# Kernel optimization log

Measured on AMD Instinct MI355X. Metric: run time of the kernel, lower is better.

## Reference

```python
import jax, jax.numpy as jnp
import numpy as np

B, N, E1, H, D = 16, 256, 4, 8, 128  # batch, max nodes, edge types+1, heads, dim
VOCAB = 100


def setup_inputs() -> dict:
    key = jax.random.key(0)
    ks = jax.random.split(key, 20)
    s = 0.05
    return dict(
        node_feat=jax.random.randint(ks[0], (B, N), 0, VOCAB),
        L=jax.random.normal(ks[1], (B, N, N, E1), jnp.float32),
        emb=jax.random.normal(ks[2], (VOCAB, D), jnp.float32) * s,
        W0=jax.random.normal(ks[3], (E1, H, D, D), jnp.float32) * s,
        W1=jax.random.normal(ks[4], (E1, H, D * H * E1, D), jnp.float32) * (s / 4.0),
        a1w0=jax.random.normal(ks[5], (E1, H, D), jnp.float32) * s,
        a1b0=jnp.zeros((E1, H), jnp.float32),
        a2w0=jax.random.normal(ks[6], (E1, H, D), jnp.float32) * s,
        a2b0=jnp.zeros((E1, H), jnp.float32),
        a1w1=jax.random.normal(ks[7], (E1, H, D), jnp.float32) * s,
        a1b1=jnp.zeros((E1, H), jnp.float32),
        a2w1=jax.random.normal(ks[8], (E1, H, D), jnp.float32) * s,
        a2b1=jnp.zeros((E1, H), jnp.float32),
        sb0=jnp.zeros((E1, H, D), jnp.float32),
        sb1=jnp.zeros((E1, H, D), jnp.float32),
        outW=jax.random.normal(ks[9], (D, D), jnp.float32) * s,
        outb=jnp.zeros((D,), jnp.float32),
        attW=jax.random.normal(ks[10], (D,), jnp.float32) * s,
        attb=jnp.zeros((), jnp.float32),
    )


def _gat_layer(state, Ltr, W, a1w, a1b, a2w, a2b, sb, last):
    # state: (B, N, Din); W: (E1, H, Din, D); Ltr: (E1, 1, B, N, N)
    Wh = jnp.einsum('bni,ehio->ehbno', state, W)                      # (E1,H,B,N,D)
    s1 = jnp.einsum('ehbno,eho->ehbn', Wh, a1w) + a1b[:, :, None, None]
    s2 = jnp.einsum('ehbno,eho->ehbn', Wh, a2w) + a2b[:, :, None, None]
    logits = jax.nn.leaky_relu(s1[..., :, None] + s2[..., None, :], 0.2) + Ltr
    att = jax.nn.softmax(logits, axis=3)  # torch softmax over dim=1 of (B,N,N)
    h = jnp.einsum('ehbnm,ehbmo->ehbno', att, Wh) + sb[:, :, None, None, :]
    if last:
        return jnp.mean(h, axis=(0, 1))                               # (B,N,D)
    h = jax.nn.elu(h)
    # concat order in torch: outer edge-type jj, inner head ii -> (B,N,E1*H*D)
    return jnp.transpose(h, (2, 3, 0, 1, 4)).reshape(state.shape[0], state.shape[1], -1)


def reference(node_feat, L, emb, W0, W1, a1w0, a1b0, a2w0, a2b0,
              a1w1, a1b1, a2w1, a2b1, sb0, sb1, outW, outb, attW, attb):
    Ltr = jnp.transpose(L, (3, 0, 1, 2))[:, None]  # (E1,1,B,N,N)
    state = emb[node_feat]                         # (B,N,D)
    state = _gat_layer(state, Ltr, W0, a1w0, a1b0, a2w0, a2b0, sb0, last=False)
    state = _gat_layer(state, Ltr, W1, a1w1, a1b1, a2w1, a2b1, sb1, last=True)
    y = state @ outW + outb                        # (B,N,D)
    aw = jax.nn.sigmoid(state @ attW + attb)       # (B,N)
    y = aw[..., None] * y
    return jnp.mean(y, axis=1)                     # (B,D)
```

## Files before the change

### kernel.cpp

```cpp
#include <hip/hip_runtime.h>
#include <hip/hip_bf16.h>

#define Bq 16
#define Nq 256
#define E1q 4
#define Hq 8
#define Dq 128
#define EH 32
#define BN 4096

typedef __hip_bfloat16 bf16;
typedef short bf16x8 __attribute__((ext_vector_type(8)));
typedef float f32x4 __attribute__((ext_vector_type(4)));

__device__ __forceinline__ void gll16(const void* gptr, void* lptr) {
    __builtin_amdgcn_global_load_lds(
        (const __attribute__((address_space(1))) void*)gptr,
        (__attribute__((address_space(3))) void*)lptr, 16, 0, 0);
}

__device__ __forceinline__ unsigned short f2bf(float v) {
    __hip_bfloat16 h = __float2bfloat16(v);
    return *(unsigned short*)&h;
}

__global__ __launch_bounds__(256) void gather_kernel(const int* __restrict__ nf,
                                                     const float* __restrict__ emb,
                                                     bf16* __restrict__ st0b) {
    int i = blockIdx.x * 256 + threadIdx.x;
    int row = i >> 7, col = i & 127;
    st0b[i] = __float2bfloat16(emb[nf[row] * Dq + col]);
}

__global__ __launch_bounds__(256) void transpose_kernel(const float* __restrict__ W,
                                                        bf16* __restrict__ WT, int K) {
    int kt = blockIdx.x, nt = blockIdx.y, eh = blockIdx.z;
    __shared__ float tile[64][65];
    int tr = threadIdx.x >> 6, tc = threadIdx.x & 63;
    const float* src = W + ((size_t)eh * K + kt * 64) * 128 + nt * 64;
#pragma unroll
    for (int p = 0; p < 16; ++p) {
        int r = p * 4 + tr;
        tile[r][tc] = src[(size_t)r * 128 + tc];
    }
    __syncthreads();
    bf16* dst = WT + ((size_t)eh * 128 + nt * 64) * K + kt * 64;
#pragma unroll
    for (int p = 0; p < 16; ++p) {
        int n = p * 4 + tr;
        dst[(size_t)n * K + tc] = __float2bfloat16(tile[tc][n]);
    }
}

__global__ __launch_bounds__(256) void pack_le_kernel(const float* __restrict__ L,
                                                      float* __restrict__ Le) {
    int idx = blockIdx.x * 256 + threadIdx.x;
    float4 v = *(const float4*)(L + (size_t)idx * 4);
    Le[idx] = v.x;
    Le[1048576 + idx] = v.y;
    Le[2097152 + idx] = v.z;
    Le[3145728 + idx] = v.w;
}

__global__ __launch_bounds__(256) void mfma_gemm_kernel(const bf16* __restrict__ Ab,
                                                        const bf16* __restrict__ Bt,
                                                        bf16* __restrict__ Wht,
                                                        const float* __restrict__ a1w,
                                                        const float* __restrict__ a1b,
                                                        const float* __restrict__ a2w,
                                                        const float* __restrict__ a2b,
                                                        float* __restrict__ s1,
                                                        float* __restrict__ s2, int K) {
    int rt = blockIdx.x;
    int eh = blockIdx.y;
    int tid = threadIdx.x;
    int w = tid >> 6, l = tid & 63;
    int q = l >> 4, mn = l & 15;
    __shared__ __align__(16) bf16 As[128 * 64];
    __shared__ __align__(16) bf16 Bs[128 * 64];
    __shared__ float red1[128], red2[128];
    const bf16* Ap = Ab + (size_t)(rt * 128) * K;
    const bf16* Bp = Bt + (size_t)eh * 128 * K;
    int lr = l >> 3;
    int g = (l & 7) ^ lr;
    int gcol = g * 8;

    if (tid < 128) { red1[tid] = 0.f; red2[tid] = 0.f; }

    f32x4 acc[4][4];
#pragma unroll
    for (int i = 0; i < 4; i++)
#pragma unroll
        for (int j = 0; j < 4; j++) acc[i][j] = (f32x4){0.f, 0.f, 0.f, 0.f};

    int wr = (w >> 1) * 64, wc = (w & 1) * 64;
    int msw = mn & 7;

    for (int k0 = 0; k0 < K; k0 += 64) {
#pragma unroll
        for (int u = 0; u < 4; ++u) {
            int i = w * 4 + u;
            int r = i * 8 + lr;
            gll16(Ap + (size_t)r * K + k0 + gcol, (char*)As + i * 1024);
            gll16(Bp + (size_t)r * K + k0 + gcol, (char*)Bs + i * 1024);
        }
        __syncthreads();
#pragma unroll
        for (int kk = 0; kk < 2; ++kk) {
            int qb = ((kk * 4 + q) ^ msw) * 16;
            bf16x8 af[4], bfr[4];
#pragma unroll
            for (int i = 0; i < 4; ++i) {
                af[i]  = *(const bf16x8*)((const char*)As + (wr + i * 16 + mn) * 128 + qb);
                bfr[i] = *(const bf16x8*)((const char*)Bs + (wc + i * 16 + mn) * 128 + qb);
            }
#pragma unroll
            for (int i = 0; i < 4; ++i)
#pragma unroll
                for (int j = 0; j < 4; ++j)
                    acc[i][j] = __builtin_amdgcn_mfma_f32_16x16x32_bf16(af[i], bfr[j], acc[i][j], 0, 0, 0);
        }
        __syncthreads();
    }
#pragma unroll
    for (int i = 0; i < 4; ++i) {
        int r0 = rt * 128 + wr + i * 16 + q * 4;
        int b = r0 >> 8, m = r0 & 255;
#pragma unroll
        for (int j = 0; j < 4; ++j) {
            int o = wc + j * 16 + mn;
            ushort4 pk;
            pk.x = f2bf(acc[i][j][0]);
            pk.y = f2bf(acc[i][j][1]);
            pk.z = f2bf(acc[i][j][2]);
            pk.w = f2bf(acc[i][j][3]);
            *(ushort4*)(Wht + ((((size_t)eh * 16 + b) * 128 + o) * 256 + m)) = pk;
        }
    }
    float w1v[4], w2v[4];
#pragma unroll
    for (int j = 0; j < 4; ++j) {
        int o = wc + j * 16 + mn;
        w1v[j] = a1w[eh * 128 + o];
        w2v[j] = a2w[eh * 128 + o];
    }
#pragma unroll
    for (int i = 0; i < 4; ++i)
#pragma unroll
        for (int r = 0; r < 4; ++r) {
            float p1 = 0.f, p2 = 0.f;
#pragma unroll
            for (int j = 0; j < 4; ++j) {
                p1 += acc[i][j][r] * w1v[j];
                p2 += acc[i][j][r] * w2v[j];
            }
#pragma unroll
            for (int off = 1; off < 16; off <<= 1) {
                p1 += __shfl_xor(p1, off);
                p2 += __shfl_xor(p2, off);
            }
            if (mn == 0) {
                int row = wr + i * 16 + q * 4 + r;
                atomicAdd(&red1[row], p1);
                atomicAdd(&red2[row], p2);
            }
        }
    __syncthreads();
    if (tid < 128) {
        int rg = rt * 128 + tid;
        s1[eh * 4096 + rg] = red1[tid] + a1b[eh];
        s2[eh * 4096 + rg] = red2[tid] + a2b[eh];
    }
}

__global__ __launch_bounds__(256) void colsoft_kernel(const float* __restrict__ s1,
                                                      const float* __restrict__ s2,
                                                      const float* __restrict__ Le,
                                                      float* __restrict__ cmax,
                                                      float* __restrict__ cinv) {
    int mt = blockIdx.x, b = blockIdx.y, e = blockIdx.z;
    int t = threadIdx.x;
    __shared__ float Lt[256 * 32];
    __shared__ float s1L[8 * 256];
#pragma unroll
    for (int i = 0; i < 8; ++i) s1L[i * 256 + t] = s1[(e * 8 + i) * 4096 + b * 256 + t];
    const float* Lb = Le + ((size_t)(e * 16 + b) * 256) * 256 + mt * 32;
#pragma unroll
    for (int j = 0; j < 8; ++j) {
        int f = t + 256 * j;
        int n = f >> 3, c4 = (f & 7) * 4;
        *(float4*)(Lt + n * 32 + c4) = *(const float4*)(Lb + (size_t)n * 256 + c4);
    }
    __syncthreads();
    int h = t >> 5, mm = t & 31;
    int m = mt * 32 + mm;
    float s2v = s2[(e * 8 + h) * 4096 + b * 256 + m];
    const float* s1p = s1L + h * 256;
    float mx = -1e30f;
    for (int n = 0; n < 256; ++n) {
        float x = s1p[n] + s2v;
        x = x > 0.f ? x : 0.2f * x;
        x += Lt[n * 32 + mm];
        mx = fmaxf(mx, x);
    }
    float sum = 0.f;
    for (int n = 0; n < 256; ++n) {
        float x = s1p[n] + s2v;
        x = x > 0.f ? x : 0.2f * x;
        x += Lt[n * 32 + mm];
        sum += __expf(x - mx);
    }
    cmax[(e * 8 + h) * 4096 + b * 256 + m] = mx;
    cinv[(e * 8 + h) * 4096 + b * 256 + m] = 1.0f / sum;
}

template <int LAST>
__global__ __launch_bounds__(256) void att_mfma_kernel(const float* __restrict__ s1,
                                                       const float* __restrict__ s2,
                                                       const float* __restrict__ cmax,
                                                       const float* __restrict__ cinv,
                                                       const float* __restrict__ Le,
                                                       const bf16* __restrict__ Wht,
                                                       const float* __restrict__ sb,
                                                       void* __restrict__ outv) {
    int nt = blockIdx.x;
    int b = blockIdx.y;
    int eh = blockIdx.z;
    int e = eh >> 3;
    int tid = threadIdx.x;
    int w = tid >> 6, l = tid & 63;
    int q = l >> 4, mn = l & 15;
    __shared__ __align__(16) bf16 As[128 * 32];
    __shared__ __align__(16) bf16 Bs[128 * 40];
    __shared__ float s1L[128], s2L[256], cmL[256], ciL[256];

    int base = eh * 4096 + b * 256;
    if (tid < 128) s1L[tid] = s1[base + nt * 128 + tid];
    s2L[tid] = s2[base + tid];
    cmL[tid] = cmax[base + tid];
    ciL[tid] = cinv[base + tid];
    __syncthreads();

    const bf16* Whtp = Wht + ((size_t)eh * 16 + b) * 32768;
    int nl = tid >> 1, mh = (tid & 1) * 16;
    const float* Lrow = Le + (((size_t)(e * 16 + b) * 256) + nt * 128 + nl) * 256;
    float s1v = s1L[nl];
    int srow = l >> 2;
    int sq = (l & 3) ^ ((l >> 3) & 3);
    int scol = sq * 8;
    int rsw = ((mn >> 1) & 3) << 3;

    f32x4 acc[4][4];
#pragma unroll
    for (int i = 0; i < 4; i++)
#pragma unroll
        for (int j = 0; j < 4; j++) acc[i][j] = (f32x4){0.f, 0.f, 0.f, 0.f};

    int wr = (w >> 1) * 64, wc = (w & 1) * 64;

    for (int k0 = 0; k0 < 256; k0 += 32) {
#pragma unroll
        for (int u = 0; u < 2; ++u) {
            int i = 2 * w + u;
            gll16(Whtp + (size_t)(i * 16 + srow) * 256 + k0 + scol, (char*)As + i * 1024);
        }
#pragma unroll
        for (int jj = 0; jj < 4; ++jj) {
            int mb = mh + jj * 4;
            float4 lv = *(const float4*)(Lrow + k0 + mb);
            float av[4];
#pragma unroll
            for (int c = 0; c < 4; ++c) {
                int m = k0 + mb + c;
                float x = s1v + s2L[m];
                x = x > 0.f ? x : 0.2f * x;
                x += ((const float*)&lv)[c];
                av[c] = __expf(x - cmL[m]) * ciL[m];
            }
            unsigned int u01 = (unsigned int)f2bf(av[0]) | ((unsigned int)f2bf(av[1]) << 16);
            unsigned int u23 = (unsigned int)f2bf(av[2]) | ((unsigned int)f2bf(av[3]) << 16);
            unsigned int* bp = (unsigned int*)Bs + (nl * 40 + mb) / 2;
            bp[0] = u01;
            bp[1] = u23;
        }
        __syncthreads();
        bf16x8 af[4], bfr[4];
#pragma unroll
        for (int i = 0; i < 4; ++i) {
            af[i]  = *(const bf16x8*)(As + (wr + i * 16 + mn) * 32 + ((q << 3) ^ rsw));
            bfr[i] = *(const bf16x8*)(Bs + (wc + i * 16 + mn) * 40 + q * 8);
        }
#pragma unroll
        for (int i = 0; i < 4; ++i)
#pragma unroll
            for (int j = 0; j < 4; ++j)
                acc[i][j] = __builtin_amdgcn_mfma_f32_16x16x32_bf16(af[i], bfr[j], acc[i][j], 0, 0, 0);
        __syncthreads();
    }
#pragma unroll
    for (int i = 0; i < 4; ++i) {
        int o0 = wr + i * 16 + q * 4;
        float4 sbv = *(const float4*)(sb + eh * 128 + o0);
#pragma unroll
        for (int j = 0; j < 4; ++j) {
            int n = wc + j * 16 + mn;
            float v0 = acc[i][j][0] + sbv.x;
            float v1 = acc[i][j][1] + sbv.y;
            float v2 = acc[i][j][2] + sbv.z;
            float v3 = acc[i][j][3] + sbv.w;
            if (LAST == 0) {
                v0 = v0 > 0.f ? v0 : __expf(v0) - 1.f;
                v1 = v1 > 0.f ? v1 : __expf(v1) - 1.f;
                v2 = v2 > 0.f ? v2 : __expf(v2) - 1.f;
                v3 = v3 > 0.f ? v3 : __expf(v3) - 1.f;
                ushort4 pk = {f2bf(v0), f2bf(v1), f2bf(v2), f2bf(v3)};
                bf16* out = (bf16*)outv;
                *(ushort4*)(out + (size_t)(b * 256 + nt * 128 + n) * 4096 + eh * 128 + o0) = pk;
            } else {
                float4 pk = {v0, v1, v2, v3};
                float* out = (float*)outv;
                *(float4*)(out + ((size_t)eh * 4096 + b * 256 + nt * 128 + n) * 128 + o0) = pk;
            }
        }
    }
}

__global__ __launch_bounds__(256) void reduce_aw_kernel(const float* __restrict__ h2,
                                                        const float* __restrict__ attW,
                                                        const float* __restrict__ attb,
                                                        float* __restrict__ st2,
                                                        float* __restrict__ aw) {
    int t = threadIdx.x;
    int rl = t >> 7, o = t & 127;
    int r = blockIdx.x * 2 + rl;
    float acc = 0.f;
#pragma unroll
    for (int eh = 0; eh < EH; ++eh) acc += h2[((size_t)eh * 4096 + r) * 128 + o];
    acc *= (1.0f / 32.0f);
    st2[(size_t)r * 128 + o] = acc;
    float p = acc * attW[o];
#pragma unroll
    for (int off = 32; off; off >>= 1) p += __shfl_down(p, off);
    __shared__ float part[4];
    if ((t & 63) == 0) part[t >> 6] = p;
    __syncthreads();
    if (t == 0) aw[r] = 1.0f / (1.0f + __expf(-(part[0] + part[1] + attb[0])));
    if (t == 128) aw[r] = 1.0f / (1.0f + __expf(-(part[2] + part[3] + attb[0])));
}

__global__ __launch_bounds__(128) void final_kernel(const float* __restrict__ st2,
                                                    const float* __restrict__ aw,
                                                    const float* __restrict__ outW,
                                                    const float* __restrict__ outb,
                                                    float* __restrict__ out) {
    int b = blockIdx.x;
    int t = threadIdx.x;
    __shared__ float awL[256], zL[128];
    awL[t] = aw[b * 256 + t];
    awL[t + 128] = aw[b * 256 + t + 128];
    __syncthreads();
    float z = 0.f;
    for (int n = 0; n < 256; ++n) z += awL[n] * st2[(size_t)(b * 256 + n) * Dq + t];
    float sa = 0.f;
    for (int n = 0; n < 256; ++n) sa += awL[n];
    zL[t] = z;
    __syncthreads();
    float acc = sa * outb[t];
    for (int o = 0; o < Dq; ++o) acc += zL[o] * outW[o * Dq + t];
    out[b * Dq + t] = acc * (1.0f / 256.0f);
}

extern "C" void kernel_launch(void* const* d_in, const int* in_sizes, int n_in,
                              void* d_out, int out_size, void* d_ws, size_t ws_size,
                              hipStream_t stream) {
    const int* nf = (const int*)d_in[0];
    const float* L = (const float*)d_in[1];
    const float* emb = (const float*)d_in[2];
    const float* W0 = (const float*)d_in[3];
    const float* W1 = (const float*)d_in[4];
    const float* a1w0 = (const float*)d_in[5];
    const float* a1b0 = (const float*)d_in[6];
    const float* a2w0 = (const float*)d_in[7];
    const float* a2b0 = (const float*)d_in[8];
    const float* a1w1 = (const float*)d_in[9];
    const float* a1b1 = (const float*)d_in[10];
    const float* a2w1 = (const float*)d_in[11];
    const float* a2b1 = (const float*)d_in[12];
    const float* sb0 = (const float*)d_in[13];
    const float* sb1 = (const float*)d_in[14];
    const float* outW = (const float*)d_in[15];
    const float* outb = (const float*)d_in[16];
    const float* attW = (const float*)d_in[17];
    const float* attb = (const float*)d_in[18];

    char* p = (char*)d_ws;
    bf16* st0b = (bf16*)(p);
    bf16* W0T  = (bf16*)(p + 1048576);
    bf16* W1T  = (bf16*)(p + 2097152);
    bf16* st1b = (bf16*)(p + 35651584);
    float* h2  = (float*)(p + 2097152);
    float* Le  = (float*)(p + 69206016);
    bf16* Wht  = (bf16*)(p + 85983232);
    float* s1  = (float*)(p + 119537664);
    float* s2  = (float*)(p + 120061952);
    float* cmax= (float*)(p + 120586240);
    float* cinv= (float*)(p + 121110528);
    float* st2 = (float*)(p);
    float* aw  = s1;
    float* outp = (float*)d_out;

    gather_kernel<<<2048, 256, 0, stream>>>(nf, emb, st0b);
    transpose_kernel<<<dim3(2, 2, 32), 256, 0, stream>>>(W0, W0T, 128);
    transpose_kernel<<<dim3(64, 2, 32), 256, 0, stream>>>(W1, W1T, 4096);
    pack_le_kernel<<<4096, 256, 0, stream>>>(L, Le);

    mfma_gemm_kernel<<<dim3(32, 32), 256, 0, stream>>>(st0b, W0T, Wht, a1w0, a1b0, a2w0, a2b0, s1, s2, 128);
    colsoft_kernel<<<dim3(8, 16, 4), 256, 0, stream>>>(s1, s2, Le, cmax, cinv);
    att_mfma_kernel<0><<<dim3(2, 16, 32), 256, 0, stream>>>(s1, s2, cmax, cinv, Le, Wht, sb0, st1b);

    mfma_gemm_kernel<<<dim3(32, 32), 256, 0, stream>>>(st1b, W1T, Wht, a1w1, a1b1, a2w1, a2b1, s1, s2, 4096);
    colsoft_kernel<<<dim3(8, 16, 4), 256, 0, stream>>>(s1, s2, Le, cmax, cinv);
    att_mfma_kernel<1><<<dim3(2, 16, 32), 256, 0, stream>>>(s1, s2, cmax, cinv, Le, Wht, sb1, h2);

    reduce_aw_kernel<<<2048, 256, 0, stream>>>(h2, attW, attb, st2, aw);
    final_kernel<<<16, 128, 0, stream>>>(st2, aw, outW, outb, outp);
}
```

Baseline: 502.1 us.

## Fuse prep kernels, remap GEMM blocks per XCD, pack softmax stats, store h2 in bf16

Merges the gather, two weight transposes and the L repack into one prep kernel to cut launch count. The GEMM grid is flattened and remapped so that blocks sharing the same weight slice land on the same XCD, which should improve L2 reuse. The s2, column max and inverse sum values are packed into one float4 array, replacing three separate loads with one. The second-layer attention output is written as bf16 instead of fp32, halving traffic into the reduction at some loss of precision.

```diff
diff --git a/kernel.cpp b/kernel.cpp
--- a/kernel.cpp
+++ b/kernel.cpp
@@ -24,19 +24,11 @@
     return *(unsigned short*)&h;
 }
 
-__global__ __launch_bounds__(256) void gather_kernel(const int* __restrict__ nf,
-                                                     const float* __restrict__ emb,
-                                                     bf16* __restrict__ st0b) {
-    int i = blockIdx.x * 256 + threadIdx.x;
-    int row = i >> 7, col = i & 127;
-    st0b[i] = __float2bfloat16(emb[nf[row] * Dq + col]);
-}
-
-__global__ __launch_bounds__(256) void transpose_kernel(const float* __restrict__ W,
-                                                        bf16* __restrict__ WT, int K) {
-    int kt = blockIdx.x, nt = blockIdx.y, eh = blockIdx.z;
-    __shared__ float tile[64][65];
-    int tr = threadIdx.x >> 6, tc = threadIdx.x & 63;
+__device__ __forceinline__ void transpose_tile(const float* __restrict__ W,
+                                               bf16* __restrict__ WT, int K,
+                                               int kt, int nt, int eh,
+                                               float (*tile)[65], int tid) {
+    int tr = tid >> 6, tc = tid & 63;
     const float* src = W + ((size_t)eh * K + kt * 64) * 128 + nt * 64;
 #pragma unroll
     for (int p = 0; p < 16; ++p) {
@@ -52,14 +44,36 @@
     }
 }
 
-__global__ __launch_bounds__(256) void pack_le_kernel(const float* __restrict__ L,
-                                                      float* __restrict__ Le) {
-    int idx = blockIdx.x * 256 + threadIdx.x;
-    float4 v = *(const float4*)(L + (size_t)idx * 4);
-    Le[idx] = v.x;
-    Le[1048576 + idx] = v.y;
-    Le[2097152 + idx] = v.z;
-    Le[3145728 + idx] = v.w;
+__global__ __launch_bounds__(256) void prep_kernel(const int* __restrict__ nf,
+                                                   const float* __restrict__ emb,
+                                                   const float* __restrict__ W0,
+                                                   const float* __restrict__ W1,
+                                                   const float* __restrict__ L,
+                                                   bf16* __restrict__ st0b,
+                                                   bf16* __restrict__ W0T,
+                                                   bf16* __restrict__ W1T,
+                                                   float* __restrict__ Le) {
+    int bid = blockIdx.x;
+    int t = threadIdx.x;
+    __shared__ float tile[64][65];
+    if (bid < 2048) {
+        int i = bid * 256 + t;
+        int row = i >> 7, col = i & 127;
+        st0b[i] = __float2bfloat16(emb[nf[row] * Dq + col]);
+    } else if (bid < 2176) {
+        int id2 = bid - 2048;
+        transpose_tile(W0, W0T, 128, id2 & 1, (id2 >> 1) & 1, id2 >> 2, tile, t);
+    } else if (bid < 6272) {
+        int id3 = bid - 2176;
+        transpose_tile(W1, W1T, 4096, id3 & 63, (id3 >> 6) & 1, id3 >> 7, tile, t);
+    } else {
+        int idx = (bid - 6272) * 256 + t;
+        float4 v = *(const float4*)(L + (size_t)idx * 4);
+        Le[idx] = v.x;
+        Le[1048576 + idx] = v.y;
+        Le[2097152 + idx] = v.z;
+        Le[3145728 + idx] = v.w;
+    }
 }
 
 __global__ __launch_bounds__(256) void mfma_gemm_kernel(const bf16* __restrict__ Ab,
@@ -71,8 +85,10 @@
                                                         const float* __restrict__ a2b,
                                                         float* __restrict__ s1,
                                                         float* __restrict__ s2, int K) {
-    int rt = blockIdx.x;
-    int eh = blockIdx.y;
+    int id = blockIdx.x;
+    int xcd = id & 7, slot = id >> 3;
+    int eh = (slot & 3) * 8 + xcd;
+    int rt = slot >> 2;
     int tid = threadIdx.x;
     int w = tid >> 6, l = tid & 63;
     int q = l >> 4, mn = l & 15;
@@ -176,8 +192,7 @@
 __global__ __launch_bounds__(256) void colsoft_kernel(const float* __restrict__ s1,
                                                       const float* __restrict__ s2,
                                                       const float* __restrict__ Le,
-                                                      float* __restrict__ cmax,
-                                                      float* __restrict__ cinv) {
+                                                      float4* __restrict__ stat) {
     int mt = blockIdx.x, b = blockIdx.y, e = blockIdx.z;
     int t = threadIdx.x;
     __shared__ float Lt[256 * 32];
@@ -210,19 +225,17 @@
         x += Lt[n * 32 + mm];
         sum += __expf(x - mx);
     }
-    cmax[(e * 8 + h) * 4096 + b * 256 + m] = mx;
-    cinv[(e * 8 + h) * 4096 + b * 256 + m] = 1.0f / sum;
+    float4 st = {s2v, mx, 1.0f / sum, 0.f};
+    stat[(e * 8 + h) * 4096 + b * 256 + m] = st;
 }
 
 template <int LAST>
 __global__ __launch_bounds__(256) void att_mfma_kernel(const float* __restrict__ s1,
-                                                       const float* __restrict__ s2,
-                                                       const float* __restrict__ cmax,
-                                                       const float* __restrict__ cinv,
+                                                       const float4* __restrict__ stat,
                                                        const float* __restrict__ Le,
                                                        const bf16* __restrict__ Wht,
                                                        const float* __restrict__ sb,
-                                                       void* __restrict__ outv) {
+                                                       bf16* __restrict__ outb) {
     int nt = blockIdx.x;
     int b = blockIdx.y;
     int eh = blockIdx.z;
@@ -232,13 +245,12 @@
     int q = l >> 4, mn = l & 15;
     __shared__ __align__(16) bf16 As[128 * 32];
     __shared__ __align__(16) bf16 Bs[128 * 40];
-    __shared__ float s1L[128], s2L[256], cmL[256], ciL[256];
+    __shared__ float s1L[128];
+    __shared__ __align__(16) float4 stL[256];
 
     int base = eh * 4096 + b * 256;
     if (tid < 128) s1L[tid] = s1[base + nt * 128 + tid];
-    s2L[tid] = s2[base + tid];
-    cmL[tid] = cmax[base + tid];
-    ciL[tid] = cinv[base + tid];
+    stL[tid] = stat[base + tid];
     __syncthreads();
 
     const bf16* Whtp = Wht + ((size_t)eh * 16 + b) * 32768;
@@ -272,10 +284,11 @@
 #pragma unroll
             for (int c = 0; c < 4; ++c) {
                 int m = k0 + mb + c;
-                float x = s1v + s2L[m];
+                float4 stv = stL[m];
+                float x = s1v + stv.x;
                 x = x > 0.f ? x : 0.2f * x;
                 x += ((const float*)&lv)[c];
-                av[c] = __expf(x - cmL[m]) * ciL[m];
+                av[c] = __expf(x - stv.y) * stv.z;
             }
             unsigned int u01 = (unsigned int)f2bf(av[0]) | ((unsigned int)f2bf(av[1]) << 16);
             unsigned int u23 = (unsigned int)f2bf(av[2]) | ((unsigned int)f2bf(av[3]) << 16);
@@ -314,18 +327,16 @@
                 v2 = v2 > 0.f ? v2 : __expf(v2) - 1.f;
                 v3 = v3 > 0.f ? v3 : __expf(v3) - 1.f;
                 ushort4 pk = {f2bf(v0), f2bf(v1), f2bf(v2), f2bf(v3)};
-                bf16* out = (bf16*)outv;
-                *(ushort4*)(out + (size_t)(b * 256 + nt * 128 + n) * 4096 + eh * 128 + o0) = pk;
+                *(ushort4*)(outb + (size_t)(b * 256 + nt * 128 + n) * 4096 + eh * Dq + o0) = pk;
             } else {
-                float4 pk = {v0, v1, v2, v3};
-                float* out = (float*)outv;
-                *(float4*)(out + ((size_t)eh * 4096 + b * 256 + nt * 128 + n) * 128 + o0) = pk;
-            }
-        }
-    }
-}
-
-__global__ __launch_bounds__(256) void reduce_aw_kernel(const float* __restrict__ h2,
+                ushort4 pk = {f2bf(v0), f2bf(v1), f2bf(v2), f2bf(v3)};
+                *(ushort4*)(outb + ((size_t)eh * 4096 + b * 256 + nt * 128 + n) * Dq + o0) = pk;
+            }
+        }
+    }
+}
+
+__global__ __launch_bounds__(256) void reduce_aw_kernel(const bf16* __restrict__ h2b,
                                                         const float* __restrict__ attW,
                                                         const float* __restrict__ attb,
                                                         float* __restrict__ st2,
@@ -335,7 +346,8 @@
     int r = blockIdx.x * 2 + rl;
     float acc = 0.f;
 #pragma unroll
-    for (int eh = 0; eh < EH; ++eh) acc += h2[((size_t)eh * 4096 + r) * 128 + o];
+    for (int eh = 0; eh < EH; ++eh)
+        acc += __bfloat162float(h2b[((size_t)eh * 4096 + r) * 128 + o]);
     acc *= (1.0f / 32.0f);
     st2[(size_t)r * 128 + o] = acc;
     float p = acc * attW[o];
@@ -398,30 +410,26 @@
     bf16* W0T  = (bf16*)(p + 1048576);
     bf16* W1T  = (bf16*)(p + 2097152);
     bf16* st1b = (bf16*)(p + 35651584);
-    float* h2  = (float*)(p + 2097152);
+    bf16* h2b  = (bf16*)(p + 2097152);
     float* Le  = (float*)(p + 69206016);
     bf16* Wht  = (bf16*)(p + 85983232);
     float* s1  = (float*)(p + 119537664);
     float* s2  = (float*)(p + 120061952);
-    float* cmax= (float*)(p + 120586240);
-    float* cinv= (float*)(p + 121110528);
+    float4* stat = (float4*)(p + 120586240);
     float* st2 = (float*)(p);
     float* aw  = s1;
     float* outp = (float*)d_out;
 
-    gather_kernel<<<2048, 256, 0, stream>>>(nf, emb, st0b);
-    transpose_kernel<<<dim3(2, 2, 32), 256, 0, stream>>>(W0, W0T, 128);
-    transpose_kernel<<<dim3(64, 2, 32), 256, 0, stream>>>(W1, W1T, 4096);
-    pack_le_kernel<<<4096, 256, 0, stream>>>(L, Le);
-
-    mfma_gemm_kernel<<<dim3(32, 32), 256, 0, stream>>>(st0b, W0T, Wht, a1w0, a1b0, a2w0, a2b0, s1, s2, 128);
-    colsoft_kernel<<<dim3(8, 16, 4), 256, 0, stream>>>(s1, s2, Le, cmax, cinv);
-    att_mfma_kernel<0><<<dim3(2, 16, 32), 256, 0, stream>>>(s1, s2, cmax, cinv, Le, Wht, sb0, st1b);
-
-    mfma_gemm_kernel<<<dim3(32, 32), 256, 0, stream>>>(st1b, W1T, Wht, a1w1, a1b1, a2w1, a2b1, s1, s2, 4096);
-    colsoft_kernel<<<dim3(8, 16, 4), 256, 0, stream>>>(s1, s2, Le, cmax, cinv);
-    att_mfma_kernel<1><<<dim3(2, 16, 32), 256, 0, stream>>>(s1, s2, cmax, cinv, Le, Wht, sb1, h2);
-
-    reduce_aw_kernel<<<2048, 256, 0, stream>>>(h2, attW, attb, st2, aw);
+    prep_kernel<<<10368, 256, 0, stream>>>(nf, emb, W0, W1, L, st0b, W0T, W1T, Le);
+
+    mfma_gemm_kernel<<<1024, 256, 0, stream>>>(st0b, W0T, Wht, a1w0, a1b0, a2w0, a2b0, s1, s2, 128);
+    colsoft_kernel<<<dim3(8, 16, 4), 256, 0, stream>>>(s1, s2, Le, stat);
+    att_mfma_kernel<0><<<dim3(2, 16, 32), 256, 0, stream>>>(s1, stat, Le, Wht, sb0, st1b);
+
+    mfma_gemm_kernel<<<1024, 256, 0, stream>>>(st1b, W1T, Wht, a1w1, a1b1, a2w1, a2b1, s1, s2, 4096);
+    colsoft_kernel<<<dim3(8, 16, 4), 256, 0, stream>>>(s1, s2, Le, stat);
+    att_mfma_kernel<1><<<dim3(2, 16, 32), 256, 0, stream>>>(s1, stat, Le, Wht, sb1, h2b);
+
+    reduce_aw_kernel<<<2048, 256, 0, stream>>>(h2b, attW, attb, st2, aw);
     final_kernel<<<16, 128, 0, stream>>>(st2, aw, outW, outb, outp);
 }
```

New measurement: 495.1 us. Within noise of the previous version (-1.4%).
